# Kernel tuning notes

Measured on AMD Instinct MI355X. Metric: run time of the kernel, lower is better.

## Reference

```python
import jax, jax.numpy as jnp
import numpy as np

B, T, C = 2, 2048, 1024
R = 16
LORA_SCALE = 1.0 / R  # lora_alpha(=1) / r


def lora_linear(x, w, b, a, bb):
    # loralib: y = x @ W^T + bias + (x @ A^T) @ B^T * scaling
    return x @ w.T + b + (x @ a.T) @ bb.T * LORA_SCALE


def setup_inputs() -> dict:
    key = jax.random.key(0)
    ks = jax.random.split(key, 8)
    s = 0.02
    return {
        "x": jax.random.normal(ks[0], (B, T, C), jnp.float32),
        "w_attn": jax.random.normal(ks[1], (3 * C, C), jnp.float32) * s,
        "b_attn": jnp.zeros((3 * C,), jnp.float32),
        "lora_a_attn": jax.random.normal(ks[2], (R, C), jnp.float32) * s,
        "lora_b_attn": jnp.zeros((3 * C, R), jnp.float32),
        "w_proj": jax.random.normal(ks[3], (C, C), jnp.float32) * s,
        "b_proj": jnp.zeros((C,), jnp.float32),
        "lora_a_proj": jax.random.normal(ks[4], (R, C), jnp.float32) * s,
        "lora_b_proj": jnp.zeros((C, R), jnp.float32),
        "n_head": 16,
    }


def reference(x, w_attn, b_attn, lora_a_attn, lora_b_attn, w_proj, b_proj,
              lora_a_proj, lora_b_proj, n_head):
    b, t, c = x.shape
    hd = c // n_head
    qkv = lora_linear(x, w_attn, b_attn, lora_a_attn, lora_b_attn)
    q, k, v = jnp.split(qkv, 3, axis=2)
    # (B, H, T, hd)
    q = q.reshape(b, t, n_head, hd).transpose(0, 2, 1, 3)
    k = k.reshape(b, t, n_head, hd).transpose(0, 2, 1, 3)
    v = v.reshape(b, t, n_head, hd).transpose(0, 2, 1, 3)
    att = jnp.einsum("bhqd,bhkd->bhqk", q, k) * (1.0 / np.sqrt(hd).astype(np.float32))
    causal = jnp.tril(jnp.ones((t, t), bool))
    att = jnp.where(causal[None, None], att, jnp.float32(-jnp.inf))
    att = jax.nn.softmax(att, axis=-1)
    y = jnp.einsum("bhqk,bhkd->bhqd", att, v)
    y = y.transpose(0, 2, 1, 3).reshape(b, t, c)
    return lora_linear(y, w_proj, b_proj, lora_a_proj, lora_b_proj)
```

## Files before the change

### kernel.cpp

```cpp
#include <hip/hip_runtime.h>

typedef __attribute__((ext_vector_type(8))) short bf16x8;
typedef __attribute__((ext_vector_type(4))) short bf16x4;
typedef __attribute__((ext_vector_type(4))) float f32x4;

__device__ __forceinline__ float bf2f(unsigned short u) {
    unsigned int x = ((unsigned int)u) << 16;
    float f;
    __builtin_memcpy(&f, &x, 4);
    return f;
}
__device__ __forceinline__ unsigned short f2bf(float f) {
    unsigned int x;
    __builtin_memcpy(&x, &f, 4);
    x += 0x7FFFu + ((x >> 16) & 1u);
    return (unsigned short)(x >> 16);
}

#define GLOAD_LDS16(gp, lp)                                      \
    __builtin_amdgcn_global_load_lds(                            \
        (const __attribute__((address_space(1))) void*)(gp),     \
        (__attribute__((address_space(3))) void*)(lp), 16, 0, 0)

__global__ __launch_bounds__(256) void prep(
    const float* __restrict__ x, unsigned short* __restrict__ xb,
    const float* __restrict__ w_attn, const float* __restrict__ la_attn,
    const float* __restrict__ lb_attn, unsigned short* __restrict__ Weff_attn,
    const float* __restrict__ w_proj, const float* __restrict__ la_proj,
    const float* __restrict__ lb_proj, unsigned short* __restrict__ Weff_proj) {
    const int bid = blockIdx.x;
    if (bid < 4096) {
        int i = (bid * 256 + threadIdx.x) * 4;
        float4 v = *(const float4*)(x + i);
        xb[i + 0] = f2bf(v.x);
        xb[i + 1] = f2bf(v.y);
        xb[i + 2] = f2bf(v.z);
        xb[i + 3] = f2bf(v.w);
        return;
    }
    const float* W;
    const float* Ain;
    const float* Bin;
    unsigned short* Weff;
    int idx;
    if (bid < 16384) {
        idx = (bid - 4096) * 256 + threadIdx.x;
        W = w_attn; Ain = la_attn; Bin = lb_attn; Weff = Weff_attn;
    } else {
        idx = (bid - 16384) * 256 + threadIdx.x;
        W = w_proj; Ain = la_proj; Bin = lb_proj; Weff = Weff_proj;
    }
    int n = idx >> 10;
    int k = idx & 1023;
    float s = 0.f;
#pragma unroll
    for (int r = 0; r < 16; ++r)
        s += Bin[n * 16 + r] * Ain[r * 1024 + k];
    Weff[idx] = f2bf(W[idx] + 0.0625f * s);
}

template <bool F32OUT, bool VSPLIT>
__global__ __launch_bounds__(256) void gemm_bt_bias(
    const unsigned short* __restrict__ A, const unsigned short* __restrict__ B,
    const float* __restrict__ bias, unsigned short* __restrict__ Cb,
    float* __restrict__ Cf, unsigned short* __restrict__ Vtout,
    int M, int N, int K) {
    __shared__ unsigned short sA[128 * 32];
    __shared__ unsigned short sB[128 * 32];
    const int tid = threadIdx.x;
    const int wave = tid >> 6, lane = tid & 63;
    const int quad = lane >> 4, l16 = lane & 15;
    const int m0 = blockIdx.y * 128, n0 = blockIdx.x * 128;
    const int wm = (wave & 1) * 64, wn = (wave >> 1) * 64;

    const int srow = wave * 32 + (lane >> 2);
    const int scol = (lane & 3) * 8;
    const unsigned short* Ag = A + (size_t)(m0 + srow) * K + scol;
    const unsigned short* Bg = B + (size_t)(n0 + srow) * K + scol;
    unsigned short* sAw = sA + wave * 1024;
    unsigned short* sBw = sB + wave * 1024;
    const size_t kjump = (size_t)16 * K;

    f32x4 acc[4][4];
#pragma unroll
    for (int i = 0; i < 4; ++i)
#pragma unroll
        for (int j = 0; j < 4; ++j) acc[i][j] = (f32x4){0.f, 0.f, 0.f, 0.f};

    for (int k0 = 0; k0 < K; k0 += 32) {
        __syncthreads();
        GLOAD_LDS16(Ag + k0, sAw);
        GLOAD_LDS16(Ag + k0 + kjump, sAw + 512);
        GLOAD_LDS16(Bg + k0, sBw);
        GLOAD_LDS16(Bg + k0 + kjump, sBw + 512);
        __syncthreads();
        bf16x8 af[4], bfr[4];
#pragma unroll
        for (int mi = 0; mi < 4; ++mi)
            af[mi] = *(const bf16x8*)&sA[(wm + mi * 16 + l16) * 32 + quad * 8];
#pragma unroll
        for (int ni = 0; ni < 4; ++ni)
            bfr[ni] = *(const bf16x8*)&sB[(wn + ni * 16 + l16) * 32 + quad * 8];
#pragma unroll
        for (int mi = 0; mi < 4; ++mi)
#pragma unroll
            for (int ni = 0; ni < 4; ++ni)
                acc[mi][ni] = __builtin_amdgcn_mfma_f32_16x16x32_bf16(
                    af[mi], bfr[ni], acc[mi][ni], 0, 0, 0);
    }
    float bv[4];
#pragma unroll
    for (int ni = 0; ni < 4; ++ni) bv[ni] = bias[n0 + wn + ni * 16 + l16];

    if (VSPLIT && n0 >= 2048) {
#pragma unroll
        for (int ni = 0; ni < 4; ++ni) {
            const int hcol = n0 + wn + ni * 16 + l16 - 2048;
#pragma unroll
            for (int mi = 0; mi < 4; ++mi) {
                const int rowtop = m0 + wm + mi * 16 + quad * 4;
                const int bb = rowtop >> 11;
                const int t = rowtop & 2047;
                bf16x4 pk;
#pragma unroll
                for (int r = 0; r < 4; ++r)
                    pk[r] = (short)f2bf(acc[mi][ni][r] + bv[ni]);
                *(bf16x4*)(Vtout +
                           ((size_t)((bb * 16 + (hcol >> 6)) * 64 + (hcol & 63))) *
                               2048 +
                           t) = pk;
            }
        }
        return;
    }

#pragma unroll
    for (int mi = 0; mi < 4; ++mi)
#pragma unroll
        for (int ni = 0; ni < 4; ++ni)
#pragma unroll
            for (int r = 0; r < 4; ++r) {
                int row = m0 + wm + mi * 16 + quad * 4 + r;
                int col = n0 + wn + ni * 16 + l16;
                float val = acc[mi][ni][r] + bv[ni];
                if (F32OUT)
                    Cf[(size_t)row * N + col] = val;
                else
                    Cb[(size_t)row * N + col] = f2bf(val);
            }
}

__global__ __launch_bounds__(256) void attn_kernel(
    const unsigned short* __restrict__ qkv,
    const unsigned short* __restrict__ Vt,
    unsigned short* __restrict__ y) {
    const int b = blockIdx.z, h = blockIdx.y;
    const int bh = b * 16 + h;
    const int qblk = (int)blockIdx.x ^ (((bh >> 3) & 1) ? 31 : 0);
    const int w = threadIdx.x >> 6, lane = threadIdx.x & 63;
    const int quad = lane >> 4, l16 = lane & 15;
    const int q0 = qblk * 64 + w * 16;
    const int ntiles = qblk + 1;

    __shared__ unsigned short sK[64 * 72];
    __shared__ unsigned short sV[64 * 72];
    __shared__ unsigned short sP[4][16 * 72];

    const unsigned short* Qb = qkv + (size_t)(b * 2048) * 3072 + h * 64;
    const unsigned short* Kg = Qb + 1024;
    const unsigned short* Vg = Vt + (size_t)(bh * 64) * 2048;

    const int rlo = threadIdx.x >> 3;
    const int c8 = (threadIdx.x & 7) * 8;

    bf16x8 qf0 = *(const bf16x8*)(Qb + (size_t)(q0 + l16) * 3072 + quad * 8);
    bf16x8 qf1 = *(const bf16x8*)(Qb + (size_t)(q0 + l16) * 3072 + 32 + quad * 8);

    f32x4 o[4];
    float lacc = 0.f;
#pragma unroll
    for (int nt = 0; nt < 4; ++nt) o[nt] = (f32x4){0.f, 0.f, 0.f, 0.f};

    const float csc = 0.125f * 1.44269504088896340736f;

    bf16x8 kr0 = *(const bf16x8*)(Kg + (size_t)rlo * 3072 + c8);
    bf16x8 kr1 = *(const bf16x8*)(Kg + (size_t)(rlo + 32) * 3072 + c8);
    bf16x8 vr0 = *(const bf16x8*)(Vg + (size_t)rlo * 2048 + c8);
    bf16x8 vr1 = *(const bf16x8*)(Vg + (size_t)(rlo + 32) * 2048 + c8);

    for (int it = 0; it < ntiles; ++it) {
        const int kv0 = it * 64;
        __syncthreads();
        *(bf16x8*)&sK[rlo * 72 + c8] = kr0;
        *(bf16x8*)&sK[(rlo + 32) * 72 + c8] = kr1;
        *(bf16x8*)&sV[rlo * 72 + c8] = vr0;
        *(bf16x8*)&sV[(rlo + 32) * 72 + c8] = vr1;
        if (it + 1 < ntiles) {
            const int nx = kv0 + 64;
            kr0 = *(const bf16x8*)(Kg + (size_t)(nx + rlo) * 3072 + c8);
            kr1 = *(const bf16x8*)(Kg + (size_t)(nx + rlo + 32) * 3072 + c8);
            vr0 = *(const bf16x8*)(Vg + (size_t)rlo * 2048 + nx + c8);
            vr1 = *(const bf16x8*)(Vg + (size_t)(rlo + 32) * 2048 + nx + c8);
        }
        __syncthreads();

        f32x4 S[4];
#pragma unroll
        for (int f = 0; f < 4; ++f) {
            bf16x8 klo = *(const bf16x8*)&sK[(f * 16 + l16) * 72 + quad * 8];
            bf16x8 khi = *(const bf16x8*)&sK[(f * 16 + l16) * 72 + 32 + quad * 8];
            S[f] = (f32x4){0.f, 0.f, 0.f, 0.f};
            S[f] = __builtin_amdgcn_mfma_f32_16x16x32_bf16(klo, qf0, S[f], 0, 0, 0);
            S[f] = __builtin_amdgcn_mfma_f32_16x16x32_bf16(khi, qf1, S[f], 0, 0, 0);
        }
        const bool diag = (it == qblk);
        const int qr16 = w * 16 + l16;
#pragma unroll
        for (int f = 0; f < 4; ++f) {
            float p0, p1, p2, p3;
            {
                float sv = S[f][0] * csc;
                asm("v_exp_f32 %0, %1" : "=v"(p0) : "v"(sv));
                sv = S[f][1] * csc;
                asm("v_exp_f32 %0, %1" : "=v"(p1) : "v"(sv));
                sv = S[f][2] * csc;
                asm("v_exp_f32 %0, %1" : "=v"(p2) : "v"(sv));
                sv = S[f][3] * csc;
                asm("v_exp_f32 %0, %1" : "=v"(p3) : "v"(sv));
            }
            if (diag) {
                int c = f * 16 + quad * 4;
                p0 = (c + 0 <= qr16) ? p0 : 0.f;
                p1 = (c + 1 <= qr16) ? p1 : 0.f;
                p2 = (c + 2 <= qr16) ? p2 : 0.f;
                p3 = (c + 3 <= qr16) ? p3 : 0.f;
            }
            lacc += (p0 + p1) + (p2 + p3);
            unsigned int d0, d1;
            asm("v_cvt_pk_bf16_f32 %0, %1, %2" : "=v"(d0) : "v"(p0), "v"(p1));
            asm("v_cvt_pk_bf16_f32 %0, %1, %2" : "=v"(d1) : "v"(p2), "v"(p3));
            *(uint2*)&sP[w][l16 * 72 + f * 16 + quad * 4] = (uint2){d0, d1};
        }
        asm volatile("" ::: "memory");
        bf16x8 pf0 = *(const bf16x8*)&sP[w][l16 * 72 + quad * 8];
        bf16x8 pf1 = *(const bf16x8*)&sP[w][l16 * 72 + 32 + quad * 8];
#pragma unroll
        for (int nt = 0; nt < 4; ++nt) {
            bf16x8 v0 = *(const bf16x8*)&sV[(nt * 16 + l16) * 72 + quad * 8];
            bf16x8 v1 = *(const bf16x8*)&sV[(nt * 16 + l16) * 72 + 32 + quad * 8];
            o[nt] = __builtin_amdgcn_mfma_f32_16x16x32_bf16(pf0, v0, o[nt], 0, 0, 0);
            o[nt] = __builtin_amdgcn_mfma_f32_16x16x32_bf16(pf1, v1, o[nt], 0, 0, 0);
        }
    }

    lacc += __shfl_xor(lacc, 16);
    lacc += __shfl_xor(lacc, 32);
    float lt[4];
#pragma unroll
    for (int r = 0; r < 4; ++r) lt[r] = __shfl(lacc, quad * 4 + r);

    unsigned short* yb = y + (size_t)(b * 2048) * 1024 + h * 64;
#pragma unroll
    for (int nt = 0; nt < 4; ++nt)
#pragma unroll
        for (int r = 0; r < 4; ++r)
            yb[(size_t)(q0 + quad * 4 + r) * 1024 + nt * 16 + l16] =
                f2bf(o[nt][r] / lt[r]);
}

extern "C" void kernel_launch(void* const* d_in, const int* in_sizes, int n_in,
                              void* d_out, int out_size, void* d_ws, size_t ws_size,
                              hipStream_t stream) {
    const float* x       = (const float*)d_in[0];
    const float* w_attn  = (const float*)d_in[1];
    const float* b_attn  = (const float*)d_in[2];
    const float* la_attn = (const float*)d_in[3];
    const float* lb_attn = (const float*)d_in[4];
    const float* w_proj  = (const float*)d_in[5];
    const float* b_proj  = (const float*)d_in[6];
    const float* la_proj = (const float*)d_in[7];
    const float* lb_proj = (const float*)d_in[8];
    float* out = (float*)d_out;

    char* w = (char*)d_ws;
    unsigned short* xb        = (unsigned short*)w; w += (size_t)4096 * 1024 * 2;
    unsigned short* Weff_attn = (unsigned short*)w; w += (size_t)3072 * 1024 * 2;
    unsigned short* Weff_proj = (unsigned short*)w; w += (size_t)1024 * 1024 * 2;
    unsigned short* qkv       = (unsigned short*)w; w += (size_t)4096 * 3072 * 2;
    unsigned short* Vt        = (unsigned short*)w; w += (size_t)32 * 64 * 2048 * 2;
    unsigned short* y         = (unsigned short*)w; w += (size_t)4096 * 1024 * 2;

    prep<<<20480, 256, 0, stream>>>(x, xb, w_attn, la_attn, lb_attn, Weff_attn,
                                    w_proj, la_proj, lb_proj, Weff_proj);
    gemm_bt_bias<false, true><<<dim3(24, 32), 256, 0, stream>>>(
        xb, Weff_attn, b_attn, qkv, (float*)nullptr, Vt, 4096, 3072, 1024);
    attn_kernel<<<dim3(32, 16, 2), 256, 0, stream>>>(qkv, Vt, y);
    gemm_bt_bias<true, false><<<dim3(8, 32), 256, 0, stream>>>(
        y, Weff_proj, b_proj, (unsigned short*)nullptr, out, (unsigned short*)nullptr,
        4096, 1024, 1024);
}
```

Before: 206.9 us.

## Add 64x128 tile GEMM for output projection and move attention barrier before prefetch

Adds a dedicated projection GEMM kernel that uses 64-row tiles instead of the original kernel's tile size. This doubles the grid to 512 blocks so more of the GPU's compute units are occupied on the 4096x1024 output projection. In the attention kernel, the second barrier now comes right after the LDS stores and before the next-tile global prefetch. That may change how the prefetch loads overlap with compute. The smaller tiles lower per-block reuse of B data in exchange for the extra parallelism.

```diff
diff --git a/kernel.cpp b/kernel.cpp
--- a/kernel.cpp
+++ b/kernel.cpp
@@ -150,6 +150,68 @@
             }
 }
 
+__global__ __launch_bounds__(256) void gemm_bt_bias64(
+    const unsigned short* __restrict__ A, const unsigned short* __restrict__ B,
+    const float* __restrict__ bias, float* __restrict__ Cf,
+    int M, int N, int K) {
+    __shared__ unsigned short sA[64 * 32];
+    __shared__ unsigned short sB[128 * 32];
+    const int tid = threadIdx.x;
+    const int wave = tid >> 6, lane = tid & 63;
+    const int quad = lane >> 4, l16 = lane & 15;
+    const int m0 = blockIdx.y * 64, n0 = blockIdx.x * 128;
+    const int wn = wave * 32;
+
+    const int srowA = wave * 16 + (lane >> 2);
+    const int srowB = wave * 32 + (lane >> 2);
+    const int scol = (lane & 3) * 8;
+    const unsigned short* Ag = A + (size_t)(m0 + srowA) * K + scol;
+    const unsigned short* Bg = B + (size_t)(n0 + srowB) * K + scol;
+    unsigned short* sAw = sA + wave * 512;
+    unsigned short* sBw = sB + wave * 1024;
+    const size_t kjump = (size_t)16 * K;
+
+    f32x4 acc[4][2];
+#pragma unroll
+    for (int i = 0; i < 4; ++i)
+#pragma unroll
+        for (int j = 0; j < 2; ++j) acc[i][j] = (f32x4){0.f, 0.f, 0.f, 0.f};
+
+    for (int k0 = 0; k0 < K; k0 += 32) {
+        __syncthreads();
+        GLOAD_LDS16(Ag + k0, sAw);
+        GLOAD_LDS16(Bg + k0, sBw);
+        GLOAD_LDS16(Bg + k0 + kjump, sBw + 512);
+        __syncthreads();
+        bf16x8 af[4], bfr[2];
+#pragma unroll
+        for (int mi = 0; mi < 4; ++mi)
+            af[mi] = *(const bf16x8*)&sA[(mi * 16 + l16) * 32 + quad * 8];
+#pragma unroll
+        for (int ni = 0; ni < 2; ++ni)
+            bfr[ni] = *(const bf16x8*)&sB[(wn + ni * 16 + l16) * 32 + quad * 8];
+#pragma unroll
+        for (int mi = 0; mi < 4; ++mi)
+#pragma unroll
+            for (int ni = 0; ni < 2; ++ni)
+                acc[mi][ni] = __builtin_amdgcn_mfma_f32_16x16x32_bf16(
+                    af[mi], bfr[ni], acc[mi][ni], 0, 0, 0);
+    }
+    float bv[2];
+#pragma unroll
+    for (int ni = 0; ni < 2; ++ni) bv[ni] = bias[n0 + wn + ni * 16 + l16];
+#pragma unroll
+    for (int mi = 0; mi < 4; ++mi)
+#pragma unroll
+        for (int ni = 0; ni < 2; ++ni)
+#pragma unroll
+            for (int r = 0; r < 4; ++r) {
+                int row = m0 + mi * 16 + quad * 4 + r;
+                int col = n0 + wn + ni * 16 + l16;
+                Cf[(size_t)row * N + col] = acc[mi][ni][r] + bv[ni];
+            }
+}
+
 __global__ __launch_bounds__(256) void attn_kernel(
     const unsigned short* __restrict__ qkv,
     const unsigned short* __restrict__ Vt,
@@ -195,6 +257,7 @@
         *(bf16x8*)&sK[(rlo + 32) * 72 + c8] = kr1;
         *(bf16x8*)&sV[rlo * 72 + c8] = vr0;
         *(bf16x8*)&sV[(rlo + 32) * 72 + c8] = vr1;
+        __syncthreads();
         if (it + 1 < ntiles) {
             const int nx = kv0 + 64;
             kr0 = *(const bf16x8*)(Kg + (size_t)(nx + rlo) * 3072 + c8);
@@ -202,7 +265,6 @@
             vr0 = *(const bf16x8*)(Vg + (size_t)rlo * 2048 + nx + c8);
             vr1 = *(const bf16x8*)(Vg + (size_t)(rlo + 32) * 2048 + nx + c8);
         }
-        __syncthreads();
 
         f32x4 S[4];
 #pragma unroll
@@ -295,7 +357,6 @@
     gemm_bt_bias<false, true><<<dim3(24, 32), 256, 0, stream>>>(
         xb, Weff_attn, b_attn, qkv, (float*)nullptr, Vt, 4096, 3072, 1024);
     attn_kernel<<<dim3(32, 16, 2), 256, 0, stream>>>(qkv, Vt, y);
-    gemm_bt_bias<true, false><<<dim3(8, 32), 256, 0, stream>>>(
-        y, Weff_proj, b_proj, (unsigned short*)nullptr, out, (unsigned short*)nullptr,
-        4096, 1024, 1024);
-}
+    gemm_bt_bias64<<<dim3(8, 64), 256, 0, stream>>>(
+        y, Weff_proj, b_proj, out, 4096, 1024, 1024);
+}
```

Result: no change. 203.2 us (-1.8%).
